# Optimization experiments

Measured on AMD Instinct MI355X. Metric: run time of the kernel, lower is better.

The kernel has to match this reference:

```python
import jax, jax.numpy as jnp
import numpy as np

D = 512       # input_dim
K = 8         # output_size (number of bilinear slices)
L = 64        # hash_length
Q = 4096      # number of query vectors
C = 4096      # number of class vectors


def setup_inputs() -> dict:
    key = jax.random.key(0)
    ks = jax.random.split(key, 8)
    class_vector = jax.random.normal(ks[0], (C, D), dtype=jnp.float32)
    query_vector = jax.random.normal(ks[1], (Q, D), dtype=jnp.float32)
    # xavier_normal over (D, D, K): std = sqrt(2 / (fan_in + fan_out))
    xav = float(np.sqrt(2.0 / (D + D)))
    M = jax.random.normal(ks[2], (D, D, K), dtype=jnp.float32) * xav
    # score_layer: Linear(K, 1)
    lim_s = 1.0 / np.sqrt(K)
    score_w = jax.random.uniform(ks[3], (K,), jnp.float32, -lim_s, lim_s)
    score_b = jax.random.uniform(ks[4], (1,), jnp.float32, -lim_s, lim_s)
    # hash_layer: Linear(D, L) + Tanh
    lim_h = 1.0 / np.sqrt(D)
    hash_w = jax.random.uniform(ks[5], (L, D), jnp.float32, -lim_h, lim_h)
    hash_b = jax.random.uniform(ks[6], (L,), jnp.float32, -lim_h, lim_h)
    return {
        "class_vector": class_vector,
        "query_vector": query_vector,
        "M": M,
        "score_w": score_w,
        "score_b": score_b,
        "hash_w": hash_w,
        "hash_b": hash_b,
    }


def reference(class_vector, query_vector, M, score_w, score_b, hash_w, hash_b):
    # Looped bilinear product fused into one einsum:
    # inter_k = Q @ (C @ M[:,:,k]).T  ->  [Q, C, K]
    bi = jnp.einsum('ci,ijk,qj->qck', class_vector, M, query_vector)
    act = jax.nn.relu(bi)
    # score_layer: Linear(K, 1) then squeeze -> [Q, C]
    other = jnp.einsum('qck,k->qc', act, score_w) + score_b[0]
    relation_scores = jax.nn.softmax(other, axis=1)       # softmax over class dim
    query_features = relation_scores @ class_vector + query_vector  # [Q, D]
    hash_codes = jnp.tanh(query_features @ hash_w.T + hash_b)       # [Q, L]
    return hash_codes
```

## Files before the change

### kernel.cpp

```cpp
#include <hip/hip_runtime.h>
#include <hip/hip_bf16.h>
#include <math.h>

#define D_ 512
#define K_ 8
#define L_ 64
#define Q_ 4096
#define C_ 4096
#define N_ (C_ * K_)

typedef short short8 __attribute__((ext_vector_type(8)));
typedef float f32x4 __attribute__((ext_vector_type(4)));

static __device__ __forceinline__ void split2(float v, unsigned short& h, unsigned short& l) {
    __hip_bfloat16 hh = __float2bfloat16(v);
    float r = v - __bfloat162float(hh);
    __hip_bfloat16 ll = __float2bfloat16(r);
    h = *reinterpret_cast<unsigned short*>(&hh);
    l = *reinterpret_cast<unsigned short*>(&ll);
}

#define ASYNC_COPY16(gp, lp)                                                        \
    __builtin_amdgcn_global_load_lds((const __attribute__((address_space(1))) void*)(gp), \
                                     (__attribute__((address_space(3))) void*)(lp), \
                                     16, 0, 0)

__global__ void transpose_M_split(const float* __restrict__ M,
                                  unsigned short* __restrict__ Mh,
                                  unsigned short* __restrict__ Ml) {
    int idx = blockIdx.x * blockDim.x + threadIdx.x;
    int i = idx & (D_ - 1);
    int n2 = idx >> 9;
    int j = n2 & (D_ - 1);
    int k = n2 >> 9;
    float v = M[((size_t)i * D_ + j) * K_ + k];
    split2(v, Mh[idx], Ml[idx]);
}

__global__ void split_f32(const float* __restrict__ x,
                          unsigned short* __restrict__ hi,
                          unsigned short* __restrict__ lo) {
    int i = blockIdx.x * blockDim.x + threadIdx.x;
    split2(x[i], hi[i], lo[i]);
}

__global__ void transpose_split_classT(const float* __restrict__ x,
                                       unsigned short* __restrict__ Th,
                                       unsigned short* __restrict__ Tl) {
    int idx = blockIdx.x * blockDim.x + threadIdx.x;
    int c = idx & (C_ - 1);
    int d = idx >> 12;
    float v = x[(size_t)c * D_ + d];
    split2(v, Th[idx], Tl[idx]);
}

#define BM 128
#define BN 128
#define BNW 32
#define BKK 32

template <int NITER>
__device__ __forceinline__ void mfma_core(
    const unsigned short* __restrict__ Agh, const unsigned short* __restrict__ Agl,
    const unsigned short* __restrict__ Bgh, const unsigned short* __restrict__ Bgl,
    int lda, int ldb, int m0, int n0,
    unsigned short (*Ahb)[BM * BKK], unsigned short (*Alb)[BM * BKK],
    f32x4 acc[8][2]) {
    const int tid = threadIdx.x;
    const int lane = tid & 63;
    const int wid = tid >> 6;
    const int fr = lane & 15;
    const int fq = lane >> 4;
    const int co = (fq ^ ((fr >> 1) & 3)) * 8;

    const unsigned short* bh0 = Bgh + (size_t)(n0 + wid * BNW + fr) * ldb + fq * 8;
    const unsigned short* bl0 = Bgl + (size_t)(n0 + wid * BNW + fr) * ldb + fq * 8;

    short8 bh[2][2], bl[2][2];

    auto stageA = [&](int buf, int j0) {
#pragma unroll
        for (int h = 0; h < 2; ++h) {
            const int i2 = h * 256 + tid;
            const int r = i2 >> 2;
            const int cg = (i2 & 3) ^ ((r >> 1) & 3);
            const int ldsoff = (h * 256 + (tid & ~63)) * 8;
            const size_t go = (size_t)(m0 + r) * lda + j0 + cg * 8;
            ASYNC_COPY16(Agh + go, &Ahb[buf][ldsoff]);
            ASYNC_COPY16(Agl + go, &Alb[buf][ldsoff]);
        }
    };
    auto loadB = [&](int buf, int j0) {
        bh[buf][0] = *(const short8*)(bh0 + j0);
        bh[buf][1] = *(const short8*)(bh0 + 16 * (size_t)ldb + j0);
        bl[buf][0] = *(const short8*)(bl0 + j0);
        bl[buf][1] = *(const short8*)(bl0 + 16 * (size_t)ldb + j0);
    };

    stageA(0, 0);
    loadB(0, 0);
    stageA(1, BKK);

#pragma unroll
    for (int it = 0; it < NITER; ++it) {
        const int cura = it % 3;
        const int curb = it & 1;
        if (it + 1 < NITER) {
            asm volatile("s_waitcnt vmcnt(4)" ::: "memory");
        } else {
            asm volatile("s_waitcnt vmcnt(0)" ::: "memory");
        }
        __builtin_amdgcn_s_barrier();
        asm volatile("" ::: "memory");
        if (it + 1 < NITER) loadB(curb ^ 1, (it + 1) * BKK);
        if (it + 2 < NITER) stageA((it + 2) % 3, (it + 2) * BKK);
#pragma unroll
        for (int mi = 0; mi < 8; ++mi) {
            const short8 ah = *(const short8*)&Ahb[cura][(mi * 16 + fr) * BKK + co];
            const short8 al = *(const short8*)&Alb[cura][(mi * 16 + fr) * BKK + co];
#pragma unroll
            for (int ni = 0; ni < 2; ++ni) {
                acc[mi][ni] = __builtin_amdgcn_mfma_f32_16x16x32_bf16(ah, bh[curb][ni], acc[mi][ni], 0, 0, 0);
                acc[mi][ni] = __builtin_amdgcn_mfma_f32_16x16x32_bf16(ah, bl[curb][ni], acc[mi][ni], 0, 0, 0);
                acc[mi][ni] = __builtin_amdgcn_mfma_f32_16x16x32_bf16(al, bh[curb][ni], acc[mi][ni], 0, 0, 0);
            }
        }
    }
}

#define CORE_PROLOGUE                                                            \
    __shared__ __attribute__((aligned(16))) unsigned short Ahb[3][BM * BKK];     \
    __shared__ __attribute__((aligned(16))) unsigned short Alb[3][BM * BKK];     \
    const int tid = threadIdx.x;                                                 \
    const int lane = tid & 63;                                                   \
    const int wid = tid >> 6;                                                    \
    const int fr = lane & 15;                                                    \
    const int fq = lane >> 4;                                                    \
    f32x4 acc[8][2] = {};                                                        \
    (void)tid;

__launch_bounds__(256, 3)
__global__ void gemm_P_mfma(const unsigned short* __restrict__ Chh,
                            const unsigned short* __restrict__ Cll,
                            const unsigned short* __restrict__ Mh,
                            const unsigned short* __restrict__ Ml,
                            unsigned short* __restrict__ Ph,
                            unsigned short* __restrict__ Pl) {
    CORE_PROLOGUE
    const int n0 = blockIdx.x * BN;
    const int c0 = blockIdx.y * BM;
    mfma_core<D_ / BKK>(Chh, Cll, Mh, Ml, D_, D_, c0, n0, Ahb, Alb, acc);
#pragma unroll
    for (int mi = 0; mi < 8; ++mi)
#pragma unroll
        for (int ni = 0; ni < 2; ++ni)
#pragma unroll
            for (int r = 0; r < 4; ++r) {
                int c = c0 + mi * 16 + fq * 4 + r;
                int n2 = n0 + wid * BNW + ni * 16 + fr;
                size_t o = (size_t)c * (K_ * D_) + n2;
                split2(acc[mi][ni][r], Ph[o], Pl[o]);
            }
}

__launch_bounds__(256, 3)
__global__ void bilinear_mfma(const unsigned short* __restrict__ Qh,
                              const unsigned short* __restrict__ Ql,
                              const unsigned short* __restrict__ Ph,
                              const unsigned short* __restrict__ Pl,
                              const float* __restrict__ sw,
                              const float* __restrict__ sb,
                              float* __restrict__ other) {
    CORE_PROLOGUE
    const int q0 = blockIdx.x * BM;
    const int n0 = blockIdx.y * BN;
    mfma_core<D_ / BKK>(Qh, Ql, Ph, Pl, D_, D_, q0, n0, Ahb, Alb, acc);
    const float wk = sw[lane & 7];
    const float bias = sb[0];
#pragma unroll
    for (int mi = 0; mi < 8; ++mi)
#pragma unroll
        for (int ni = 0; ni < 2; ++ni)
#pragma unroll
            for (int r = 0; r < 4; ++r) {
                float v = wk * fmaxf(acc[mi][ni][r], 0.f);
                v += __shfl_xor(v, 1);
                v += __shfl_xor(v, 2);
                v += __shfl_xor(v, 4);
                if ((lane & 7) == 0) {
                    int q = q0 + mi * 16 + fq * 4 + r;
                    int c = (n0 + wid * BNW + ni * 16 + fr) >> 3;
                    other[(size_t)q * C_ + c] = v + bias;
                }
            }
}

__launch_bounds__(256, 3)
__global__ void gemm_qf_mfma(const unsigned short* __restrict__ Sh,
                             const unsigned short* __restrict__ Sl,
                             const unsigned short* __restrict__ Th,
                             const unsigned short* __restrict__ Tl,
                             float* __restrict__ qfp_base) {
    CORE_PROLOGUE
    const int n0 = blockIdx.x * BN;
    const int q0 = blockIdx.y * BM;
    const int zoff = blockIdx.z * (C_ / 8);
    float* qfp = qfp_base + (size_t)blockIdx.z * Q_ * D_;
    mfma_core<(C_ / 8) / BKK>(Sh + zoff, Sl + zoff, Th + zoff, Tl + zoff,
                              C_, C_, q0, n0, Ahb, Alb, acc);
#pragma unroll
    for (int mi = 0; mi < 8; ++mi)
#pragma unroll
        for (int ni = 0; ni < 2; ++ni)
#pragma unroll
            for (int r = 0; r < 4; ++r) {
                int q = q0 + mi * 16 + fq * 4 + r;
                int d = n0 + wid * BNW + ni * 16 + fr;
                qfp[(size_t)q * D_ + d] = acc[mi][ni][r];
            }
}

__launch_bounds__(256)
__global__ void softmax_split(const float* __restrict__ other,
                              unsigned short* __restrict__ Sh,
                              unsigned short* __restrict__ Sl) {
    const int q = blockIdx.x;
    const float* row = other + (size_t)q * C_;
    const int tid = threadIdx.x;
    __shared__ float red[4];
    float v[16];
    float m = -1e30f;
#pragma unroll
    for (int it = 0; it < 16; ++it) {
        v[it] = row[tid + it * 256];
        m = fmaxf(m, v[it]);
    }
#pragma unroll
    for (int off = 32; off; off >>= 1) m = fmaxf(m, __shfl_down(m, off));
    if ((tid & 63) == 0) red[tid >> 6] = m;
    __syncthreads();
    m = fmaxf(fmaxf(red[0], red[1]), fmaxf(red[2], red[3]));
    __syncthreads();
    float s = 0.f;
#pragma unroll
    for (int it = 0; it < 16; ++it) {
        v[it] = __expf(v[it] - m);
        s += v[it];
    }
#pragma unroll
    for (int off = 32; off; off >>= 1) s += __shfl_down(s, off);
    if ((tid & 63) == 0) red[tid >> 6] = s;
    __syncthreads();
    const float inv = 1.f / (red[0] + red[1] + red[2] + red[3]);
#pragma unroll
    for (int it = 0; it < 16; ++it) {
        size_t o = (size_t)q * C_ + tid + it * 256;
        split2(v[it] * inv, Sh[o], Sl[o]);
    }
}

__launch_bounds__(256)
__global__ void hash_kernel(const float* __restrict__ qfp_base,
                            const float* __restrict__ Qv,
                            const float* __restrict__ hw,
                            const float* __restrict__ hb,
                            float* __restrict__ out) {
    __shared__ float sqf[4 * D_];
    const int q0 = blockIdx.x * 4;
    const int tid = threadIdx.x;
    {
        float4* dst = (float4*)sqf;
#pragma unroll
        for (int it = 0; it < 2; ++it) {
            int i = tid + it * 256;
            const float4* sq = (const float4*)&Qv[(size_t)q0 * D_];
            float4 o = sq[i];
#pragma unroll
            for (int z = 0; z < 8; ++z) {
                const float4* sz = (const float4*)&qfp_base[(size_t)z * Q_ * D_ + q0 * D_];
                float4 a = sz[i];
                o.x += a.x; o.y += a.y; o.z += a.z; o.w += a.w;
            }
            dst[i] = o;
        }
    }
    __syncthreads();
    const int l = tid % L_;
    const int qi = tid / L_;
    float s = hb[l];
    const float* wrow = &hw[(size_t)l * D_];
    const float* xrow = &sqf[qi * D_];
#pragma unroll 4
    for (int d = 0; d < D_; d += 4) {
        float4 w4 = *(const float4*)&wrow[d];
        float4 x4 = *(const float4*)&xrow[d];
        s += x4.x * w4.x + x4.y * w4.y + x4.z * w4.z + x4.w * w4.w;
    }
    out[(size_t)(q0 + qi) * L_ + l] = tanhf(s);
}

extern "C" void kernel_launch(void* const* d_in, const int* in_sizes, int n_in,
                              void* d_out, int out_size, void* d_ws, size_t ws_size,
                              hipStream_t stream) {
    const float* class_v = (const float*)d_in[0];
    const float* query_v = (const float*)d_in[1];
    const float* M       = (const float*)d_in[2];
    const float* score_w = (const float*)d_in[3];
    const float* score_b = (const float*)d_in[4];
    const float* hash_w  = (const float*)d_in[5];
    const float* hash_b  = (const float*)d_in[6];
    float* out = (float*)d_out;

    char* base = (char*)d_ws;
    unsigned short* Ph = (unsigned short*)base;
    unsigned short* Pl = (unsigned short*)(base + (size_t)33554432);
    char* oreg          = base + (size_t)67108864;
    float* other        = (float*)oreg;
    unsigned short* Mh  = (unsigned short*)oreg;
    unsigned short* Ml  = (unsigned short*)(oreg + (size_t)4194304);
    unsigned short* Chh = (unsigned short*)(oreg + (size_t)8388608);
    unsigned short* Cll = (unsigned short*)(oreg + (size_t)12582912);
    float* qfp          = (float*)oreg;
    char* scratch = base + (size_t)134217728;
    unsigned short* Qh = (unsigned short*)scratch;
    unsigned short* Ql = (unsigned short*)(scratch + (size_t)4194304);
    unsigned short* Th = (unsigned short*)scratch;
    unsigned short* Tl = (unsigned short*)(scratch + (size_t)4194304);
    unsigned short* Sh = Ph;
    unsigned short* Sl = Pl;

    transpose_M_split<<<(K_ * D_ * D_) / 256, 256, 0, stream>>>(M, Mh, Ml);
    split_f32<<<(C_ * D_) / 256, 256, 0, stream>>>(class_v, Chh, Cll);
    split_f32<<<(Q_ * D_) / 256, 256, 0, stream>>>(query_v, Qh, Ql);
    gemm_P_mfma<<<dim3((K_ * D_) / BN, C_ / BM), 256, 0, stream>>>(Chh, Cll, Mh, Ml, Ph, Pl);
    bilinear_mfma<<<dim3(Q_ / BM, N_ / BN), 256, 0, stream>>>(Qh, Ql, Ph, Pl,
                                                              score_w, score_b, other);
    softmax_split<<<Q_, 256, 0, stream>>>(other, Sh, Sl);
    transpose_split_classT<<<(C_ * D_) / 256, 256, 0, stream>>>(class_v, Th, Tl);
    gemm_qf_mfma<<<dim3(D_ / BN, Q_ / BM, 8), 256, 0, stream>>>(Sh, Sl, Th, Tl, qfp);
    hash_kernel<<<Q_ / 4, 256, 0, stream>>>(qfp, query_v, hash_w, hash_b, out);
}
```

Before: 759.8 us.

## Use LDS-tiled transposes and double-buffered MFMA pipeline with higher occupancy

The two transpose-and-split kernels now stage 64x64 tiles in shared memory, so both global reads and writes are coalesced where before one side was strided. The GEMM core drops from a triple-buffered async A pipeline with explicit vmcnt waits to a double-buffered scheme with __syncthreads after each iteration. Shared memory use per block falls, and launch bounds rise from 3 to 5 blocks per CU. The simpler pipeline gives less load/compute overlap per block and adds a full barrier per k-step, in exchange for more resident blocks to hide latency.

```diff
diff --git a/kernel.cpp b/kernel.cpp
--- a/kernel.cpp
+++ b/kernel.cpp
@@ -28,13 +28,26 @@
 __global__ void transpose_M_split(const float* __restrict__ M,
                                   unsigned short* __restrict__ Mh,
                                   unsigned short* __restrict__ Ml) {
-    int idx = blockIdx.x * blockDim.x + threadIdx.x;
-    int i = idx & (D_ - 1);
-    int n2 = idx >> 9;
-    int j = n2 & (D_ - 1);
-    int k = n2 >> 9;
-    float v = M[((size_t)i * D_ + j) * K_ + k];
-    split2(v, Mh[idx], Ml[idx]);
+    __shared__ float tile[64][65];
+    const int tid = threadIdx.x;
+    const int jk0 = blockIdx.x * 64;
+    const int i0  = blockIdx.y * 64;
+    const int c = tid & 63, r4 = tid >> 6;
+#pragma unroll
+    for (int p = 0; p < 16; ++p) {
+        int ii = p * 4 + r4;
+        tile[ii][c] = M[(size_t)(i0 + ii) * 4096 + jk0 + c];
+    }
+    __syncthreads();
+#pragma unroll
+    for (int p = 0; p < 16; ++p) {
+        int jj = p * 4 + r4;
+        int jk = jk0 + jj;
+        int n = (jk & 7) * 512 + (jk >> 3);
+        float v = tile[c][jj];
+        size_t o = (size_t)n * 512 + i0 + c;
+        split2(v, Mh[o], Ml[o]);
+    }
 }
 
 __global__ void split_f32(const float* __restrict__ x,
@@ -47,11 +60,24 @@
 __global__ void transpose_split_classT(const float* __restrict__ x,
                                        unsigned short* __restrict__ Th,
                                        unsigned short* __restrict__ Tl) {
-    int idx = blockIdx.x * blockDim.x + threadIdx.x;
-    int c = idx & (C_ - 1);
-    int d = idx >> 12;
-    float v = x[(size_t)c * D_ + d];
-    split2(v, Th[idx], Tl[idx]);
+    __shared__ float tile[64][65];
+    const int tid = threadIdx.x;
+    const int d0 = blockIdx.x * 64;
+    const int c0 = blockIdx.y * 64;
+    const int c = tid & 63, r4 = tid >> 6;
+#pragma unroll
+    for (int p = 0; p < 16; ++p) {
+        int cc = p * 4 + r4;
+        tile[cc][c] = x[(size_t)(c0 + cc) * 512 + d0 + c];
+    }
+    __syncthreads();
+#pragma unroll
+    for (int p = 0; p < 16; ++p) {
+        int dd = p * 4 + r4;
+        float v = tile[c][dd];
+        size_t o = (size_t)(d0 + dd) * 4096 + c0 + c;
+        split2(v, Th[o], Tl[o]);
+    }
 }
 
 #define BM 128
@@ -99,38 +125,33 @@
 
     stageA(0, 0);
     loadB(0, 0);
-    stageA(1, BKK);
+    __syncthreads();
 
 #pragma unroll
     for (int it = 0; it < NITER; ++it) {
-        const int cura = it % 3;
-        const int curb = it & 1;
+        const int cur = it & 1, nxt = cur ^ 1;
         if (it + 1 < NITER) {
-            asm volatile("s_waitcnt vmcnt(4)" ::: "memory");
-        } else {
-            asm volatile("s_waitcnt vmcnt(0)" ::: "memory");
+            stageA(nxt, (it + 1) * BKK);
+            loadB(nxt, (it + 1) * BKK);
         }
-        __builtin_amdgcn_s_barrier();
-        asm volatile("" ::: "memory");
-        if (it + 1 < NITER) loadB(curb ^ 1, (it + 1) * BKK);
-        if (it + 2 < NITER) stageA((it + 2) % 3, (it + 2) * BKK);
 #pragma unroll
         for (int mi = 0; mi < 8; ++mi) {
-            const short8 ah = *(const short8*)&Ahb[cura][(mi * 16 + fr) * BKK + co];
-            const short8 al = *(const short8*)&Alb[cura][(mi * 16 + fr) * BKK + co];
+            const short8 ah = *(const short8*)&Ahb[cur][(mi * 16 + fr) * BKK + co];
+            const short8 al = *(const short8*)&Alb[cur][(mi * 16 + fr) * BKK + co];
 #pragma unroll
             for (int ni = 0; ni < 2; ++ni) {
-                acc[mi][ni] = __builtin_amdgcn_mfma_f32_16x16x32_bf16(ah, bh[curb][ni], acc[mi][ni], 0, 0, 0);
-                acc[mi][ni] = __builtin_amdgcn_mfma_f32_16x16x32_bf16(ah, bl[curb][ni], acc[mi][ni], 0, 0, 0);
-                acc[mi][ni] = __builtin_amdgcn_mfma_f32_16x16x32_bf16(al, bh[curb][ni], acc[mi][ni], 0, 0, 0);
+                acc[mi][ni] = __builtin_amdgcn_mfma_f32_16x16x32_bf16(ah, bh[cur][ni], acc[mi][ni], 0, 0, 0);
+                acc[mi][ni] = __builtin_amdgcn_mfma_f32_16x16x32_bf16(ah, bl[cur][ni], acc[mi][ni], 0, 0, 0);
+                acc[mi][ni] = __builtin_amdgcn_mfma_f32_16x16x32_bf16(al, bh[cur][ni], acc[mi][ni], 0, 0, 0);
             }
         }
+        __syncthreads();
     }
 }
 
 #define CORE_PROLOGUE                                                            \
-    __shared__ __attribute__((aligned(16))) unsigned short Ahb[3][BM * BKK];     \
-    __shared__ __attribute__((aligned(16))) unsigned short Alb[3][BM * BKK];     \
+    __shared__ __attribute__((aligned(16))) unsigned short Ahb[2][BM * BKK];     \
+    __shared__ __attribute__((aligned(16))) unsigned short Alb[2][BM * BKK];     \
     const int tid = threadIdx.x;                                                 \
     const int lane = tid & 63;                                                   \
     const int wid = tid >> 6;                                                    \
@@ -139,7 +160,7 @@
     f32x4 acc[8][2] = {};                                                        \
     (void)tid;
 
-__launch_bounds__(256, 3)
+__launch_bounds__(256, 5)
 __global__ void gemm_P_mfma(const unsigned short* __restrict__ Chh,
                             const unsigned short* __restrict__ Cll,
                             const unsigned short* __restrict__ Mh,
@@ -163,7 +184,7 @@
             }
 }
 
-__launch_bounds__(256, 3)
+__launch_bounds__(256, 5)
 __global__ void bilinear_mfma(const unsigned short* __restrict__ Qh,
                               const unsigned short* __restrict__ Ql,
                               const unsigned short* __restrict__ Ph,
@@ -195,7 +216,7 @@
             }
 }
 
-__launch_bounds__(256, 3)
+__launch_bounds__(256, 5)
 __global__ void gemm_qf_mfma(const unsigned short* __restrict__ Sh,
                              const unsigned short* __restrict__ Sl,
                              const unsigned short* __restrict__ Th,
@@ -329,14 +350,14 @@
     unsigned short* Sh = Ph;
     unsigned short* Sl = Pl;
 
-    transpose_M_split<<<(K_ * D_ * D_) / 256, 256, 0, stream>>>(M, Mh, Ml);
+    transpose_M_split<<<dim3(64, 8), 256, 0, stream>>>(M, Mh, Ml);
     split_f32<<<(C_ * D_) / 256, 256, 0, stream>>>(class_v, Chh, Cll);
     split_f32<<<(Q_ * D_) / 256, 256, 0, stream>>>(query_v, Qh, Ql);
     gemm_P_mfma<<<dim3((K_ * D_) / BN, C_ / BM), 256, 0, stream>>>(Chh, Cll, Mh, Ml, Ph, Pl);
     bilinear_mfma<<<dim3(Q_ / BM, N_ / BN), 256, 0, stream>>>(Qh, Ql, Ph, Pl,
                                                               score_w, score_b, other);
     softmax_split<<<Q_, 256, 0, stream>>>(other, Sh, Sl);
-    transpose_split_classT<<<(C_ * D_) / 256, 256, 0, stream>>>(class_v, Th, Tl);
+    transpose_split_classT<<<dim3(8, 64), 256, 0, stream>>>(class_v, Th, Tl);
     gemm_qf_mfma<<<dim3(D_ / BN, Q_ / BM, 8), 256, 0, stream>>>(Sh, Sl, Th, Tl, qfp);
     hash_kernel<<<Q_ / 4, 256, 0, stream>>>(qfp, query_v, hash_w, hash_b, out);
 }
```

Measured after the change: 1.420 ms. 1.87x slower.
